# Kernel optimization log

Hardware: AMD Instinct MI355X
Metric: run time of the kernel (lower is better)

The kernel has to match this reference:

```python
import jax, jax.numpy as jnp
import numpy as np

B, T, D, H = 64, 196, 768, 3072
WBIT_MAX = 127.0          # int8 symmetric weight range
BIAS_MAX = 2.0 ** 31 - 1  # bias_bit = 32


def round_ste(v):
    # straight-through rounding (QAT semantics)
    return v + jax.lax.stop_gradient(jnp.round(v) - v)


def quant_linear(x, w, b, a_s, relu_clip):
    # symmetric per-tensor int8 weight quantization
    w_s = jnp.max(jnp.abs(w)) / WBIT_MAX
    w_int = jnp.clip(round_ste(w / w_s), -WBIT_MAX, WBIT_MAX)
    # bias quantized at the accumulator scale a_s * w_s (int32 range)
    b_int = jnp.clip(round_ste(b / (w_s * a_s)), -BIAS_MAX, BIAS_MAX)
    out = jnp.einsum('btd,hd->bth', x, w_int) + b_int  # integer-domain accumulation
    if relu_clip:
        out = jax.nn.relu(out)
    return out, w_s, a_s * w_s


def setup_inputs() -> dict:
    key = jax.random.key(0)
    ks = jax.random.split(key, 6)
    x = jnp.round(jax.random.normal(ks[0], (B, T, D), dtype=jnp.float32) * 20.0)  # int8-like activations
    w1 = jax.random.normal(ks[1], (H, D), dtype=jnp.float32) * 0.02
    b1 = jax.random.normal(ks[2], (H,), dtype=jnp.float32) * 0.02
    w2 = jax.random.normal(ks[3], (D, H), dtype=jnp.float32) * 0.02
    b2 = jax.random.normal(ks[4], (D,), dtype=jnp.float32) * 0.02
    a_s = jax.random.uniform(ks[5], (1,), dtype=jnp.float32, minval=0.01, maxval=0.05)
    return {"x": x, "w1": w1, "b1": b1, "w2": w2, "b2": b2, "a_s": a_s}


def reference(x, w1, b1, w2, b2, a_s):
    s = a_s[0]
    # fc1: quantized linear, no activation clip
    h, w_s1, s = quant_linear(x, w1, b1, s, relu_clip=False)
    # fc2: quantized linear with ReLU clip
    out, w_s2, s = quant_linear(h, w2, b2, s, relu_clip=True)
    return (out, s)
```

## Files before the change

kernel.cpp:

```cpp
#include <hip/hip_runtime.h>
#include <hip/hip_bf16.h>
#include <type_traits>

typedef __attribute__((ext_vector_type(8))) short bf16x8;
typedef __attribute__((ext_vector_type(4))) float f32x4;
typedef __attribute__((ext_vector_type(4))) int   i32x4;

static __device__ __forceinline__ unsigned short f2bf(float f) {
  union { float f; unsigned u; } cv; cv.f = f;
  unsigned r = cv.u + 0x7fff + ((cv.u >> 16) & 1);
  return (unsigned short)(r >> 16);
}

static __device__ __forceinline__ void stage16(const void* g, void* l) {
  __builtin_amdgcn_global_load_lds((const __attribute__((address_space(1))) void*)g,
                                   (__attribute__((address_space(3))) void*)l,
                                   16, 0, 0);
}

__global__ void prep_kernel(const float4* __restrict__ x, uchar4* __restrict__ xq, int n4x,
                            const float4* __restrict__ w1, const float4* __restrict__ w2,
                            int n4w, unsigned* __restrict__ mx) {
  if (blockIdx.y == 0) {
    const int stride = gridDim.x * blockDim.x;
    for (int i = blockIdx.x * blockDim.x + threadIdx.x; i < n4x; i += stride) {
      float4 v = x[i];
      uchar4 o;
      o.x = (unsigned char)(char)fminf(fmaxf(v.x, -127.f), 127.f);
      o.y = (unsigned char)(char)fminf(fmaxf(v.y, -127.f), 127.f);
      o.z = (unsigned char)(char)fminf(fmaxf(v.z, -127.f), 127.f);
      o.w = (unsigned char)(char)fminf(fmaxf(v.w, -127.f), 127.f);
      xq[i] = o;
    }
  } else {
    if (blockIdx.x >= 96) return;
    __shared__ unsigned red[4];
    const float4* w = (blockIdx.y == 1) ? w1 : w2;
    unsigned m = 0;
    const int stride = 96 * 256;
    for (int i = blockIdx.x * blockDim.x + threadIdx.x; i < n4w; i += stride) {
      float4 v = w[i];
      unsigned a;
      a = __float_as_uint(fabsf(v.x)); m = m > a ? m : a;
      a = __float_as_uint(fabsf(v.y)); m = m > a ? m : a;
      a = __float_as_uint(fabsf(v.z)); m = m > a ? m : a;
      a = __float_as_uint(fabsf(v.w)); m = m > a ? m : a;
    }
#pragma unroll
    for (int off = 32; off > 0; off >>= 1) {
      unsigned t = (unsigned)__shfl_down((int)m, off, 64);
      m = m > t ? m : t;
    }
    if ((threadIdx.x & 63) == 0) red[threadIdx.x >> 6] = m;
    __syncthreads();
    if (threadIdx.x == 0) {
      unsigned t0 = red[0] > red[1] ? red[0] : red[1];
      unsigned t1 = red[2] > red[3] ? red[2] : red[3];
      atomicMax(mx + blockIdx.y - 1, t0 > t1 ? t0 : t1);
    }
  }
}

__global__ void scales_bias_kernel(const unsigned* __restrict__ mx, const float* __restrict__ a_s,
                                   const float* __restrict__ b1, const float* __restrict__ b2,
                                   float* __restrict__ sc, float* __restrict__ s_out,
                                   float* __restrict__ b1i, float* __restrict__ b2i,
                                   int H, int D) {
  float ws1 = __uint_as_float(mx[0]) / 127.0f;
  float ws2 = __uint_as_float(mx[1]) / 127.0f;
  float s0 = a_s[0];
  float s1 = s0 * ws1;
  float d1 = ws1 * s0;
  float d2 = ws2 * s1;
  if (threadIdx.x == 0) {
    sc[0] = ws1;
    sc[1] = ws2;
    s_out[0] = s1 * ws2;
  }
  for (int i = threadIdx.x; i < H; i += blockDim.x) {
    float q = rintf(b1[i] / d1);
    b1i[i] = fminf(fmaxf(q, -2147483647.f), 2147483647.f);
  }
  for (int i = threadIdx.x; i < D; i += blockDim.x) {
    float q = rintf(b2[i] / d2);
    b2i[i] = fminf(fmaxf(q, -2147483647.f), 2147483647.f);
  }
}

__global__ void quantw2_kernel(const float4* __restrict__ w1, const float4* __restrict__ w2,
                               uchar4* __restrict__ w1q, ushort4* __restrict__ w2q,
                               const float* __restrict__ sc, int n4) {
  float ws = sc[blockIdx.y];
  int stride = gridDim.x * blockDim.x;
  if (blockIdx.y == 0) {
    for (int i = blockIdx.x * blockDim.x + threadIdx.x; i < n4; i += stride) {
      float4 v = w1[i];
      uchar4 o;
      o.x = (unsigned char)(char)fminf(fmaxf(rintf(v.x / ws), -127.f), 127.f);
      o.y = (unsigned char)(char)fminf(fmaxf(rintf(v.y / ws), -127.f), 127.f);
      o.z = (unsigned char)(char)fminf(fmaxf(rintf(v.z / ws), -127.f), 127.f);
      o.w = (unsigned char)(char)fminf(fmaxf(rintf(v.w / ws), -127.f), 127.f);
      w1q[i] = o;
    }
  } else {
    for (int i = blockIdx.x * blockDim.x + threadIdx.x; i < n4; i += stride) {
      float4 v = w2[i];
      ushort4 o;
      o.x = f2bf(fminf(fmaxf(rintf(v.x / ws), -127.f), 127.f));
      o.y = f2bf(fminf(fmaxf(rintf(v.y / ws), -127.f), 127.f));
      o.z = f2bf(fminf(fmaxf(rintf(v.z / ws), -127.f), 127.f));
      o.w = f2bf(fminf(fmaxf(rintf(v.w / ws), -127.f), 127.f));
      w2q[i] = o;
    }
  }
}


template<int MODE>
__global__ __launch_bounds__(256) void gemm_d(
    const char* __restrict__ A,
    const char* __restrict__ Bt,
    const float* __restrict__ bias,
    void* __restrict__ Cout,
    int M, int N, int Kb)
{
  __shared__ char lds[2 * 32768];
  const int tid = threadIdx.x;
  const int lane = tid & 63;
  const int wave = tid >> 6;
  const int wr = wave >> 1;
  const int wc = wave & 1;

  const int nbx = M / 128;
  const int nby = N / 128;
  int r, c;
  if (MODE == 0) {
    const int bandSize = 16 * nby;
    const int b = blockIdx.x / bandSize;
    const int local = blockIdx.x - b * bandSize;
    const int r0 = b * 16;
    const int rn = min(16, nbx - r0);
    c = local / rn;
    r = r0 + (local - c * rn);
  } else {
    const int nwg = nbx * nby;
    const int q8 = nwg >> 3, r8 = nwg & 7;
    const int xcd = blockIdx.x & 7, bidx = blockIdx.x >> 3;
    const int wg = (xcd < r8 ? xcd * (q8 + 1) : r8 * (q8 + 1) + (xcd - r8) * q8) + bidx;
    r = wg / nby;
    c = wg % nby;
  }
  const int row0 = r * 128;
  const int col0 = c * 128;

  const int srow = tid >> 3;
  const int chunk = (tid & 7) ^ (srow & 7);
  const char* Ag = A + (size_t)(row0 + srow) * Kb + chunk * 16;
  const char* Bg = Bt + (size_t)(col0 + srow) * Kb + chunk * 16;
  const int stA = wave * 1024;
  const int stB = 16384 + wave * 1024;

  auto stage = [&](int slot, int h) {
    const int hb = h << 7;
    char* da = lds + slot * 32768 + stA;
    char* db = lds + slot * 32768 + stB;
#pragma unroll
    for (int i = 0; i < 4; ++i)
      stage16(Ag + hb + (size_t)(i * 32) * Kb, da + i * 4096);
#pragma unroll
    for (int i = 0; i < 4; ++i)
      stage16(Bg + hb + (size_t)(i * 32) * Kb, db + i * 4096);
  };

  using accv = typename std::conditional<MODE == 0, i32x4, f32x4>::type;
  using frag = typename std::conditional<MODE == 0, i32x4, bf16x8>::type;
  accv acc[4][4];
#pragma unroll
  for (int i = 0; i < 4; ++i)
#pragma unroll
    for (int j = 0; j < 4; ++j) acc[i][j] = (accv)(0);

  const int nS = Kb >> 7;
  stage(0, 0);
  stage(1, 1);
  asm volatile("s_waitcnt vmcnt(8)" ::: "memory");
  __builtin_amdgcn_s_barrier();

  const int fr = lane & 15;
  const int fg = lane >> 4;
  const int xw = (fg ^ (fr & 7)) << 4;
  const int aoff = (wr * 64 + fr) * 128 + xw;
  const int boff = 16384 + (wc * 64 + fr) * 128 + xw;

  for (int t = 0; t < nS; ++t) {
    const int so = (t & 1) * 32768;
    frag af[2][4], bf[2][4];
#pragma unroll
    for (int h = 0; h < 2; ++h) {
      const int hx = h << 6;
#pragma unroll
      for (int mi = 0; mi < 4; ++mi)
        af[h][mi] = *(const frag*)(lds + so + ((aoff ^ hx) + mi * 2048));
#pragma unroll
      for (int ni = 0; ni < 4; ++ni)
        bf[h][ni] = *(const frag*)(lds + so + ((boff ^ hx) + ni * 2048));
    }
    asm volatile("s_waitcnt lgkmcnt(0)" ::: "memory");
    __builtin_amdgcn_sched_barrier(0);
    __builtin_amdgcn_s_barrier();
    if (t + 2 < nS) stage(t & 1, t + 2);
    __builtin_amdgcn_s_setprio(1);
#pragma unroll
    for (int h = 0; h < 2; ++h)
#pragma unroll
      for (int mi = 0; mi < 4; ++mi)
#pragma unroll
        for (int ni = 0; ni < 4; ++ni) {
          if (MODE == 0)
            acc[mi][ni] = __builtin_amdgcn_mfma_i32_16x16x64_i8(
                (i32x4)af[h][mi], (i32x4)bf[h][ni], (i32x4)acc[mi][ni], 0, 0, 0);
          else
            acc[mi][ni] = __builtin_amdgcn_mfma_f32_16x16x32_bf16(
                (bf16x8)af[h][mi], (bf16x8)bf[h][ni], (f32x4)acc[mi][ni], 0, 0, 0);
        }
    __builtin_amdgcn_s_setprio(0);
    if (t + 2 < nS) asm volatile("s_waitcnt vmcnt(8)" ::: "memory");
    else            asm volatile("s_waitcnt vmcnt(0)" ::: "memory");
    __builtin_amdgcn_s_barrier();
  }

  const int orow = row0 + wr * 64 + fg * 4;
  const int ocol = col0 + wc * 64 + fr;
#pragma unroll
  for (int mi = 0; mi < 4; ++mi) {
#pragma unroll
    for (int ni = 0; ni < 4; ++ni) {
      const int col = ocol + ni * 16;
      const float bv = bias[col];
#pragma unroll
      for (int rg = 0; rg < 4; ++rg) {
        const size_t idx = (size_t)(orow + mi * 16 + rg) * N + col;
        if (MODE == 0) {
          float v = (float)((i32x4)acc[mi][ni])[rg] + bv;
          ((unsigned short*)Cout)[idx] = f2bf(v);
        } else {
          float v = ((f32x4)acc[mi][ni])[rg] + bv;
          ((float*)Cout)[idx] = fmaxf(v, 0.f);
        }
      }
    }
  }
}


extern "C" void kernel_launch(void* const* d_in, const int* in_sizes, int n_in,
                              void* d_out, int out_size, void* d_ws, size_t ws_size,
                              hipStream_t stream) {
  const float* x  = (const float*)d_in[0];
  const float* w1 = (const float*)d_in[1];
  const float* b1 = (const float*)d_in[2];
  const float* w2 = (const float*)d_in[3];
  const float* b2 = (const float*)d_in[4];
  const float* as = (const float*)d_in[5];

  const int Mrows = 64 * 196;
  const int D = 768, H = 3072;

  char* ws = (char*)d_ws;
  size_t off = 0;
  auto align256 = [](size_t v) { return (v + 255) & ~(size_t)255; };
  unsigned* mx = (unsigned*)(ws + off); off += 256;
  float* sc    = (float*)(ws + off);    off += 256;
  char* xq8    = (char*)(ws + off);     off += align256((size_t)Mrows * D);
  char* w1q8   = (char*)(ws + off);     off += align256((size_t)H * D);
  unsigned short* w2q = (unsigned short*)(ws + off); off += align256((size_t)D * H * 2);
  float* b1i = (float*)(ws + off); off += align256((size_t)H * 4);
  float* b2i = (float*)(ws + off); off += align256((size_t)D * 4);
  unsigned short* h = (unsigned short*)(ws + off); off += align256((size_t)Mrows * H * 2);
  if (off > ws_size) return;

  float* out = (float*)d_out;
  float* s_out = out + (out_size - 1);

  hipMemsetAsync(mx, 0, 8, stream);

  const int nw4 = H * D / 4;
  prep_kernel<<<dim3(1024, 3), dim3(256), 0, stream>>>(
      (const float4*)x, (uchar4*)xq8, Mrows * D / 4,
      (const float4*)w1, (const float4*)w2, nw4, mx);
  scales_bias_kernel<<<dim3(1), dim3(256), 0, stream>>>(mx, as, b1, b2, sc, s_out, b1i, b2i, H, D);
  quantw2_kernel<<<dim3(1024, 2), dim3(256), 0, stream>>>(
      (const float4*)w1, (const float4*)w2, (uchar4*)w1q8, (ushort4*)w2q, sc, nw4);

  gemm_d<0><<<dim3((Mrows / 128) * (H / 128)), dim3(256), 0, stream>>>(
      xq8, w1q8, b1i, h, Mrows, H, D);
  gemm_d<1><<<dim3((Mrows / 128) * (D / 128)), dim3(256), 0, stream>>>(
      (const char*)h, (const char*)w2q, b2i, out, Mrows, D, H * 2);
}
```

Before: 149.4 us.

## Use 3-stage 64-byte K pipeline in GEMMs and fuse scale/bias prep kernel

The GEMM main loop now uses 64-byte K steps with a triple-buffered LDS ring (48KB) instead of 128-byte steps double-buffered in 64KB. The barrier before issuing the next stage is removed, and launch bounds request 3 blocks per CU. The goal is more latency hiding and occupancy. The scales/bias kernel is folded into the weight quantization kernel as an extra grid row, which removes one launch. The trade-off is more loop iterations and barriers per tile and a new swizzle pattern that must avoid LDS bank conflicts.

```diff
diff --git a/kernel.cpp b/kernel.cpp
--- a/kernel.cpp
+++ b/kernel.cpp
@@ -61,70 +61,61 @@
   }
 }
 
-__global__ void scales_bias_kernel(const unsigned* __restrict__ mx, const float* __restrict__ a_s,
-                                   const float* __restrict__ b1, const float* __restrict__ b2,
-                                   float* __restrict__ sc, float* __restrict__ s_out,
-                                   float* __restrict__ b1i, float* __restrict__ b2i,
-                                   int H, int D) {
-  float ws1 = __uint_as_float(mx[0]) / 127.0f;
-  float ws2 = __uint_as_float(mx[1]) / 127.0f;
-  float s0 = a_s[0];
-  float s1 = s0 * ws1;
-  float d1 = ws1 * s0;
-  float d2 = ws2 * s1;
-  if (threadIdx.x == 0) {
-    sc[0] = ws1;
-    sc[1] = ws2;
-    s_out[0] = s1 * ws2;
-  }
-  for (int i = threadIdx.x; i < H; i += blockDim.x) {
-    float q = rintf(b1[i] / d1);
-    b1i[i] = fminf(fmaxf(q, -2147483647.f), 2147483647.f);
-  }
-  for (int i = threadIdx.x; i < D; i += blockDim.x) {
-    float q = rintf(b2[i] / d2);
-    b2i[i] = fminf(fmaxf(q, -2147483647.f), 2147483647.f);
-  }
-}
-
-__global__ void quantw2_kernel(const float4* __restrict__ w1, const float4* __restrict__ w2,
+__global__ void quantwb_kernel(const float4* __restrict__ w1, const float4* __restrict__ w2,
                                uchar4* __restrict__ w1q, ushort4* __restrict__ w2q,
-                               const float* __restrict__ sc, int n4) {
-  float ws = sc[blockIdx.y];
-  int stride = gridDim.x * blockDim.x;
+                               const float* __restrict__ b1, const float* __restrict__ b2,
+                               float* __restrict__ b1i, float* __restrict__ b2i,
+                               const unsigned* __restrict__ mx, const float* __restrict__ a_s,
+                               float* __restrict__ s_out, int n4, int H, int D) {
+  const float ws1 = __uint_as_float(mx[0]) / 127.0f;
+  const float ws2 = __uint_as_float(mx[1]) / 127.0f;
+  const int stride = gridDim.x * blockDim.x;
   if (blockIdx.y == 0) {
     for (int i = blockIdx.x * blockDim.x + threadIdx.x; i < n4; i += stride) {
       float4 v = w1[i];
       uchar4 o;
-      o.x = (unsigned char)(char)fminf(fmaxf(rintf(v.x / ws), -127.f), 127.f);
-      o.y = (unsigned char)(char)fminf(fmaxf(rintf(v.y / ws), -127.f), 127.f);
-      o.z = (unsigned char)(char)fminf(fmaxf(rintf(v.z / ws), -127.f), 127.f);
-      o.w = (unsigned char)(char)fminf(fmaxf(rintf(v.w / ws), -127.f), 127.f);
+      o.x = (unsigned char)(char)fminf(fmaxf(rintf(v.x / ws1), -127.f), 127.f);
+      o.y = (unsigned char)(char)fminf(fmaxf(rintf(v.y / ws1), -127.f), 127.f);
+      o.z = (unsigned char)(char)fminf(fmaxf(rintf(v.z / ws1), -127.f), 127.f);
+      o.w = (unsigned char)(char)fminf(fmaxf(rintf(v.w / ws1), -127.f), 127.f);
       w1q[i] = o;
     }
-  } else {
+  } else if (blockIdx.y == 1) {
     for (int i = blockIdx.x * blockDim.x + threadIdx.x; i < n4; i += stride) {
       float4 v = w2[i];
       ushort4 o;
-      o.x = f2bf(fminf(fmaxf(rintf(v.x / ws), -127.f), 127.f));
-      o.y = f2bf(fminf(fmaxf(rintf(v.y / ws), -127.f), 127.f));
-      o.z = f2bf(fminf(fmaxf(rintf(v.z / ws), -127.f), 127.f));
-      o.w = f2bf(fminf(fmaxf(rintf(v.w / ws), -127.f), 127.f));
+      o.x = f2bf(fminf(fmaxf(rintf(v.x / ws2), -127.f), 127.f));
+      o.y = f2bf(fminf(fmaxf(rintf(v.y / ws2), -127.f), 127.f));
+      o.z = f2bf(fminf(fmaxf(rintf(v.z / ws2), -127.f), 127.f));
+      o.w = f2bf(fminf(fmaxf(rintf(v.w / ws2), -127.f), 127.f));
       w2q[i] = o;
     }
+  } else {
+    if (blockIdx.x != 0) return;
+    const float s0 = a_s[0];
+    const float s1 = s0 * ws1;
+    const float d1 = ws1 * s0;
+    const float d2 = ws2 * s1;
+    if (threadIdx.x == 0) s_out[0] = s1 * ws2;
+    for (int i = threadIdx.x; i < H; i += blockDim.x) {
+      float q = rintf(b1[i] / d1);
+      b1i[i] = fminf(fmaxf(q, -2147483647.f), 2147483647.f);
+    }
+    for (int i = threadIdx.x; i < D; i += blockDim.x) {
+      float q = rintf(b2[i] / d2);
+      b2i[i] = fminf(fmaxf(q, -2147483647.f), 2147483647.f);
+    }
   }
 }
 
 
 template<int MODE>
-__global__ __launch_bounds__(256) void gemm_d(
-    const char* __restrict__ A,
-    const char* __restrict__ Bt,
-    const float* __restrict__ bias,
-    void* __restrict__ Cout,
+static __device__ __forceinline__ void gemm_core(
+    char* lds,
+    const char* __restrict__ A, const char* __restrict__ Bt,
+    const float* __restrict__ bias, void* __restrict__ Cout,
     int M, int N, int Kb)
 {
-  __shared__ char lds[2 * 32768];
   const int tid = threadIdx.x;
   const int lane = tid & 63;
   const int wave = tid >> 6;
@@ -153,23 +144,19 @@
   const int row0 = r * 128;
   const int col0 = c * 128;
 
-  const int srow = tid >> 3;
-  const int chunk = (tid & 7) ^ (srow & 7);
+  const int srow = tid >> 2;
+  const int chunk = (tid & 3) ^ ((tid >> 3) & 3);
   const char* Ag = A + (size_t)(row0 + srow) * Kb + chunk * 16;
   const char* Bg = Bt + (size_t)(col0 + srow) * Kb + chunk * 16;
-  const int stA = wave * 1024;
-  const int stB = 16384 + wave * 1024;
-
-  auto stage = [&](int slot, int h) {
-    const int hb = h << 7;
-    char* da = lds + slot * 32768 + stA;
-    char* db = lds + slot * 32768 + stB;
-#pragma unroll
-    for (int i = 0; i < 4; ++i)
-      stage16(Ag + hb + (size_t)(i * 32) * Kb, da + i * 4096);
-#pragma unroll
-    for (int i = 0; i < 4; ++i)
-      stage16(Bg + hb + (size_t)(i * 32) * Kb, db + i * 4096);
+  const int wb = wave * 1024;
+
+  auto stage = [&](int slot, int st) {
+    char* base = lds + slot * 16384;
+    const int ko = st * 64;
+    stage16(Ag + ko, base + wb);
+    stage16(Ag + ko + (size_t)64 * Kb, base + 4096 + wb);
+    stage16(Bg + ko, base + 8192 + wb);
+    stage16(Bg + ko + (size_t)64 * Kb, base + 12288 + wb);
   };
 
   using accv = typename std::conditional<MODE == 0, i32x4, f32x4>::type;
@@ -180,53 +167,48 @@
 #pragma unroll
     for (int j = 0; j < 4; ++j) acc[i][j] = (accv)(0);
 
-  const int nS = Kb >> 7;
+  const int nS = Kb >> 6;
   stage(0, 0);
   stage(1, 1);
-  asm volatile("s_waitcnt vmcnt(8)" ::: "memory");
+  asm volatile("s_waitcnt vmcnt(4)" ::: "memory");
   __builtin_amdgcn_s_barrier();
 
   const int fr = lane & 15;
   const int fg = lane >> 4;
-  const int xw = (fg ^ (fr & 7)) << 4;
-  const int aoff = (wr * 64 + fr) * 128 + xw;
-  const int boff = 16384 + (wc * 64 + fr) * 128 + xw;
-
+  const int xw = (fg ^ ((fr >> 1) & 3)) << 4;
+  const int aoff = (wr * 64 + fr) * 64 + xw;
+  const int boff = 8192 + (wc * 64 + fr) * 64 + xw;
+
+  int rs = 0, ss = 2;
   for (int t = 0; t < nS; ++t) {
-    const int so = (t & 1) * 32768;
-    frag af[2][4], bf[2][4];
-#pragma unroll
-    for (int h = 0; h < 2; ++h) {
-      const int hx = h << 6;
-#pragma unroll
-      for (int mi = 0; mi < 4; ++mi)
-        af[h][mi] = *(const frag*)(lds + so + ((aoff ^ hx) + mi * 2048));
-#pragma unroll
-      for (int ni = 0; ni < 4; ++ni)
-        bf[h][ni] = *(const frag*)(lds + so + ((boff ^ hx) + ni * 2048));
-    }
-    asm volatile("s_waitcnt lgkmcnt(0)" ::: "memory");
-    __builtin_amdgcn_sched_barrier(0);
-    __builtin_amdgcn_s_barrier();
-    if (t + 2 < nS) stage(t & 1, t + 2);
+    const int so = rs << 14;
+    frag af[4], bf[4];
+#pragma unroll
+    for (int mi = 0; mi < 4; ++mi) af[mi] = *(const frag*)(lds + so + aoff + mi * 1024);
+#pragma unroll
+    for (int ni = 0; ni < 4; ++ni) bf[ni] = *(const frag*)(lds + so + boff + ni * 1024);
+    const bool st = (t + 2 < nS);
+    if (st) stage(ss, t + 2);
     __builtin_amdgcn_s_setprio(1);
 #pragma unroll
-    for (int h = 0; h < 2; ++h)
-#pragma unroll
-      for (int mi = 0; mi < 4; ++mi)
-#pragma unroll
-        for (int ni = 0; ni < 4; ++ni) {
-          if (MODE == 0)
-            acc[mi][ni] = __builtin_amdgcn_mfma_i32_16x16x64_i8(
-                (i32x4)af[h][mi], (i32x4)bf[h][ni], (i32x4)acc[mi][ni], 0, 0, 0);
-          else
-            acc[mi][ni] = __builtin_amdgcn_mfma_f32_16x16x32_bf16(
-                (bf16x8)af[h][mi], (bf16x8)bf[h][ni], (f32x4)acc[mi][ni], 0, 0, 0);
-        }
+    for (int mi = 0; mi < 4; ++mi)
+#pragma unroll
+      for (int ni = 0; ni < 4; ++ni) {
+        if (MODE == 0)
+          acc[mi][ni] = __builtin_amdgcn_mfma_i32_16x16x64_i8(
+              (i32x4)af[mi], (i32x4)bf[ni], (i32x4)acc[mi][ni], 0, 0, 0);
+        else
+          acc[mi][ni] = __builtin_amdgcn_mfma_f32_16x16x32_bf16(
+              (bf16x8)af[mi], (bf16x8)bf[ni], (f32x4)acc[mi][ni], 0, 0, 0);
+      }
     __builtin_amdgcn_s_setprio(0);
-    if (t + 2 < nS) asm volatile("s_waitcnt vmcnt(8)" ::: "memory");
-    else            asm volatile("s_waitcnt vmcnt(0)" ::: "memory");
-    __builtin_amdgcn_s_barrier();
+    if (t + 1 < nS) {
+      if (st) asm volatile("s_waitcnt vmcnt(4)" ::: "memory");
+      else    asm volatile("s_waitcnt vmcnt(0)" ::: "memory");
+      __builtin_amdgcn_s_barrier();
+    }
+    rs = (rs == 2) ? 0 : rs + 1;
+    ss = (ss == 2) ? 0 : ss + 1;
   }
 
   const int orow = row0 + wr * 64 + fg * 4;
@@ -252,6 +234,20 @@
   }
 }
 
+__global__ __launch_bounds__(256, 3) void gemm_fc1(
+    const char* __restrict__ A, const char* __restrict__ Bt,
+    const float* __restrict__ bias, void* __restrict__ Cout, int M, int N, int Kb) {
+  __shared__ char lds[49152];
+  gemm_core<0>(lds, A, Bt, bias, Cout, M, N, Kb);
+}
+
+__global__ __launch_bounds__(256, 3) void gemm_fc2(
+    const char* __restrict__ A, const char* __restrict__ Bt,
+    const float* __restrict__ bias, void* __restrict__ Cout, int M, int N, int Kb) {
+  __shared__ char lds[49152];
+  gemm_core<1>(lds, A, Bt, bias, Cout, M, N, Kb);
+}
+
 
 extern "C" void kernel_launch(void* const* d_in, const int* in_sizes, int n_in,
                               void* d_out, int out_size, void* d_ws, size_t ws_size,
@@ -270,7 +266,6 @@
   size_t off = 0;
   auto align256 = [](size_t v) { return (v + 255) & ~(size_t)255; };
   unsigned* mx = (unsigned*)(ws + off); off += 256;
-  float* sc    = (float*)(ws + off);    off += 256;
   char* xq8    = (char*)(ws + off);     off += align256((size_t)Mrows * D);
   char* w1q8   = (char*)(ws + off);     off += align256((size_t)H * D);
   unsigned short* w2q = (unsigned short*)(ws + off); off += align256((size_t)D * H * 2);
@@ -288,12 +283,12 @@
   prep_kernel<<<dim3(1024, 3), dim3(256), 0, stream>>>(
       (const float4*)x, (uchar4*)xq8, Mrows * D / 4,
       (const float4*)w1, (const float4*)w2, nw4, mx);
-  scales_bias_kernel<<<dim3(1), dim3(256), 0, stream>>>(mx, as, b1, b2, sc, s_out, b1i, b2i, H, D);
-  quantw2_kernel<<<dim3(1024, 2), dim3(256), 0, stream>>>(
-      (const float4*)w1, (const float4*)w2, (uchar4*)w1q8, (ushort4*)w2q, sc, nw4);
-
-  gemm_d<0><<<dim3((Mrows / 128) * (H / 128)), dim3(256), 0, stream>>>(
+  quantwb_kernel<<<dim3(1024, 3), dim3(256), 0, stream>>>(
+      (const float4*)w1, (const float4*)w2, (uchar4*)w1q8, (ushort4*)w2q,
+      b1, b2, b1i, b2i, mx, as, s_out, nw4, H, D);
+
+  gemm_fc1<<<dim3((Mrows / 128) * (H / 128)), dim3(256), 0, stream>>>(
       xq8, w1q8, b1i, h, Mrows, H, D);
-  gemm_d<1><<<dim3((Mrows / 128) * (D / 128)), dim3(256), 0, stream>>>(
+  gemm_fc2<<<dim3((Mrows / 128) * (D / 128)), dim3(256), 0, stream>>>(
       (const char*)h, (const char*)w2q, b2i, out, Mrows, D, H * 2);
 }
```

New measurement: 158.1 us. 1.06x slower.
